# Kernel tuning notes

Hardware: AMD Instinct MI355X
Metric: run time of the kernel (lower is better)

Reference implementation:

```python
import jax, jax.numpy as jnp
import numpy as np

T, B, E, H, V, L = 128, 64, 1024, 1024, 10000, 2


def setup_inputs() -> dict:
    key = jax.random.key(0)
    ks = jax.random.split(key, 10)
    k = 1.0 / np.sqrt(H)
    u = lambda kk, shape, a: jax.random.uniform(kk, shape, jnp.float32, -a, a)
    return {
        "emb_table": u(ks[0], (V, E), 0.1),
        "W_in0": u(ks[1], (H, E), k),   # first layer input weight (no bias in linear_W)
        "Wh0": u(ks[2], (H, H), k),
        "b0": u(ks[3], (H,), k),
        "W_in1": u(ks[4], (H, H), k),
        "Wh1": u(ks[5], (H, H), k),
        "b1": u(ks[6], (H,), k),
        "Wdec": u(ks[7], (V, H), 0.1),
        "bdec": jnp.zeros((V,), jnp.float32),
        "hidden": jnp.zeros((L, B, H), jnp.float32),
        "tokens": jax.random.randint(ks[8], (T, B), 0, V, jnp.int32),
    }


def reference(emb_table, W_in0, Wh0, b0, W_in1, Wh1, b1, Wdec, bdec, hidden, tokens):
    # dp_keep_prob = 1.0 -> dropout is identity
    x_emb = emb_table[tokens]  # [T, B, E]

    def step(h, x):
        # h: [L, B, H]; x: [B, E]
        h0 = jnp.tanh(x @ W_in0.T + h[0] @ Wh0.T + b0)
        h1 = jnp.tanh(h0 @ W_in1.T + h[1] @ Wh1.T + b1)
        logits_t = h1 @ Wdec.T + bdec  # [B, V]
        return jnp.stack([h0, h1]), logits_t

    h_final, logits = jax.lax.scan(step, hidden, x_emb)
    return logits, h_final  # [T, B, V], [L, B, H]
```

## Files before the change

kernel.cpp:

```cpp
#include <hip/hip_runtime.h>
#include <hip/hip_bf16.h>
#include <stdint.h>

typedef __bf16 bf16_t;
typedef __bf16 bf16x8 __attribute__((ext_vector_type(8)));
typedef __bf16 bf16x4 __attribute__((ext_vector_type(4)));
typedef float  floatx4 __attribute__((ext_vector_type(4)));

#define T_STEPS 128
#define BATCH   64
#define EDIM    1024
#define HDIM    1024
#define VOCAB   10000
#define MROWS   (T_STEPS * BATCH)
#define RNN_BLOCKS 128
#define BH      (BATCH * HDIM)

__device__ __forceinline__ floatx4 mfma16(bf16x8 a, bf16x8 b, floatx4 c) {
    return __builtin_amdgcn_mfma_f32_16x16x32_bf16(a, b, c, 0, 0, 0);
}

__device__ __forceinline__ void gl_lds16(const bf16_t* g, bf16_t* l) {
    __builtin_amdgcn_global_load_lds(
        (const __attribute__((address_space(1))) void*)g,
        (__attribute__((address_space(3))) void*)l, 16, 0, 0);
}

__device__ __forceinline__ void store_bf16_bypass(bf16_t* p, float v) {
    union { bf16_t b; unsigned short u; } cv;
    cv.b = (bf16_t)v;
    unsigned int d = cv.u;
    asm volatile("global_store_short %0, %1, off sc0 sc1"
                 :: "v"(p), "v"(d) : "memory");
}


__global__ void f2b_kernel(const float* __restrict__ s, bf16_t* __restrict__ d, int n) {
    int i = (blockIdx.x * blockDim.x + threadIdx.x) * 4;
    if (i < n) {
        float4 v = *(const float4*)(s + i);
        bf16x4 o;
        o.x = (bf16_t)v.x; o.y = (bf16_t)v.y; o.z = (bf16_t)v.z; o.w = (bf16_t)v.w;
        *(bf16x4*)(d + i) = o;
    }
}

__global__ void gather_kernel(const float* __restrict__ emb, const int* __restrict__ tok,
                              bf16_t* __restrict__ X) {
    int row = blockIdx.x;
    int t = tok[row];
    int e = threadIdx.x * 4;
    float4 v = *(const float4*)(emb + (size_t)t * EDIM + e);
    bf16x4 o;
    o.x = (bf16_t)v.x; o.y = (bf16_t)v.y; o.z = (bf16_t)v.z; o.w = (bf16_t)v.w;
    *(bf16x4*)(X + (size_t)row * EDIM + e) = o;
}

__global__ void init_state_kernel(const float* __restrict__ hidden,
                                  bf16_t* __restrict__ h0all, bf16_t* __restrict__ h1all,
                                  int* __restrict__ flags) {
    int i = blockIdx.x * blockDim.x + threadIdx.x;
    h0all[i] = (bf16_t)hidden[i];
    h1all[i] = (bf16_t)hidden[BATCH * HDIM + i];
    if (i < 128) flags[i] = 0;
}


template <int OUT_BF16>
__global__ __launch_bounds__(256) void gemm_kernel(
    const bf16_t* __restrict__ A, const bf16_t* __restrict__ W,
    const float* __restrict__ bias, void* __restrict__ out,
    int M, int N, int K)
{
    const int tid  = threadIdx.x;
    const int lane = tid & 63;
    const int wave = tid >> 6;
    const int wm   = wave & 1;
    const int wn   = wave >> 1;
    const int quad = lane >> 4;
    const int l16  = lane & 15;
    const int mTile = blockIdx.y * 128;
    const int nTile = blockIdx.x * 128;

    __shared__ __align__(16) bf16_t sA[128 * 32];
    __shared__ __align__(16) bf16_t sW[128 * 32];

    const floatx4 fzero = {0.f, 0.f, 0.f, 0.f};
    floatx4 acc[4][4];
    #pragma unroll
    for (int i = 0; i < 4; ++i)
        #pragma unroll
        for (int j = 0; j < 4; ++j) acc[i][j] = fzero;

    for (int kk = 0; kk < K; kk += 32) {
        __syncthreads();
        #pragma unroll
        for (int j = 0; j < 2; ++j) {
            int c   = tid + j * 256;
            int row = c >> 2;
            int sub = c & 3;
            gl_lds16(A + (size_t)(mTile + row) * K + kk + sub * 8, sA + c * 8);
            int wrow = nTile + row;
            if (wrow >= N) wrow = N - 1;
            gl_lds16(W + (size_t)wrow * K + kk + sub * 8, sW + c * 8);
        }
        __syncthreads();
        bf16x8 af[4], wf[4];
        #pragma unroll
        for (int mi = 0; mi < 4; ++mi)
            af[mi] = *(const bf16x8*)(sA + (wm * 64 + mi * 16 + l16) * 32 + quad * 8);
        #pragma unroll
        for (int ni = 0; ni < 4; ++ni)
            wf[ni] = *(const bf16x8*)(sW + (wn * 64 + ni * 16 + l16) * 32 + quad * 8);
        #pragma unroll
        for (int mi = 0; mi < 4; ++mi)
            #pragma unroll
            for (int ni = 0; ni < 4; ++ni)
                acc[mi][ni] = mfma16(af[mi], wf[ni], acc[mi][ni]);
    }

    #pragma unroll
    for (int ni = 0; ni < 4; ++ni) {
        int col = nTile + wn * 64 + ni * 16 + l16;
        if (col < N) {
            float bv = bias[col];
            #pragma unroll
            for (int mi = 0; mi < 4; ++mi) {
                #pragma unroll
                for (int r = 0; r < 4; ++r) {
                    int row = mTile + wm * 64 + mi * 16 + quad * 4 + r;
                    float v = acc[mi][ni][r] + bv;
                    if (OUT_BF16) ((bf16_t*)out)[(size_t)row * N + col] = (bf16_t)v;
                    else          ((float*)out)[(size_t)row * N + col] = v;
                }
            }
        }
    }
}


__global__ __launch_bounds__(256, 1) void rnn_step_kernel(
    const bf16_t* __restrict__ X0,
    const bf16_t* __restrict__ Wh0b,
    const bf16_t* __restrict__ Win1b,
    const bf16_t* __restrict__ Wh1b,
    const float*  __restrict__ b1,
    bf16_t* __restrict__ h0all,
    bf16_t* __restrict__ h1all,
    int* __restrict__ flags)
{
    __shared__ __align__(16) char smem[65536];
    const int tid  = threadIdx.x;
    const int lane = tid & 63;
    const int wave = tid >> 6;
    const int quad = lane >> 4;
    const int l16  = lane & 15;
    const bool isL1 = blockIdx.x >= 64;
    const int cb    = blockIdx.x & 63;
    const int cbase = cb * 16;
    const int colg  = cbase + l16;
    const int arow  = (wave * 16 + l16) * HDIM;
    const int orow0 = wave * 16 + quad * 4;
    const floatx4 fzero = {0.f, 0.f, 0.f, 0.f};
    int* f0 = flags;
    int* f1 = flags + 64;

    {
        const bf16_t* W0 = isL1 ? Win1b : Wh0b;
        for (int c = tid; c < 2048; c += 256) {
            int kc2 = c >> 6, ln = c & 63;
            const bf16_t* src = W0 + (size_t)(cbase + (ln & 15)) * HDIM + kc2 * 32 + (ln >> 4) * 8;
            *(int4*)(smem + c * 16) = *(const int4*)src;
        }
        if (isL1) {
            for (int c = tid; c < 2048; c += 256) {
                int kc2 = c >> 6, ln = c & 63;
                const bf16_t* src = Wh1b + (size_t)(cbase + (ln & 15)) * HDIM + kc2 * 32 + (ln >> 4) * 8;
                *(int4*)(smem + 32768 + c * 16) = *(const int4*)src;
            }
        }
    }
    __syncthreads();

    if (!isL1) {
        float xr[4];
        #pragma unroll
        for (int r = 0; r < 4; ++r)
            xr[r] = (float)X0[(size_t)(orow0 + r) * HDIM + colg];
        int vc = 0;
        for (int t = 0; t < T_STEPS; ++t) {
            if (t > 0) {
                if (wave == 0) {
                    while (!__all(vc >= t)) {
                        if (vc < t)
                            vc = __hip_atomic_load(&f0[lane], __ATOMIC_RELAXED,
                                                   __HIP_MEMORY_SCOPE_AGENT);
                    }
                }
                __syncthreads();
            }
            const bf16_t* Ap = h0all + (size_t)t * BH;
            bf16x8 av[32];
            #pragma unroll
            for (int kc = 0; kc < 32; ++kc)
                av[kc] = *(const bf16x8*)(Ap + arow + kc * 32 + quad * 8);
            float xn[4];
            if (t + 1 < T_STEPS) {
                #pragma unroll
                for (int r = 0; r < 4; ++r)
                    xn[r] = (float)X0[((size_t)(t + 1) * BATCH + orow0 + r) * HDIM + colg];
            }
            floatx4 a0 = fzero, a1 = fzero;
            #pragma unroll
            for (int kc = 0; kc < 32; ++kc) {
                bf16x8 wv = *(const bf16x8*)(smem + kc * 1024 + lane * 16);
                if (kc & 1) a1 = mfma16(av[kc], wv, a1);
                else        a0 = mfma16(av[kc], wv, a0);
            }
            bf16_t* dst = h0all + (size_t)(t + 1) * BH;
            #pragma unroll
            for (int r = 0; r < 4; ++r)
                store_bf16_bypass(dst + (size_t)(orow0 + r) * HDIM + colg,
                                  tanhf(xr[r] + a0[r] + a1[r]));
            #pragma unroll
            for (int r = 0; r < 4; ++r) xr[r] = xn[r];
            asm volatile("s_waitcnt vmcnt(0)" ::: "memory");
            __syncthreads();
            if (tid == 0)
                __hip_atomic_store(&f0[cb], t + 1, __ATOMIC_RELAXED,
                                   __HIP_MEMORY_SCOPE_AGENT);
        }
    } else {
        const float bb = b1[colg];
        int vc0 = 0, vc1 = 0;
        for (int t = 0; t < T_STEPS; ++t) {
            if (wave == 0) {
                while (!__all(vc0 >= t + 1)) {
                    if (vc0 < t + 1)
                        vc0 = __hip_atomic_load(&f0[lane], __ATOMIC_RELAXED,
                                                __HIP_MEMORY_SCOPE_AGENT);
                }
            }
            __syncthreads();
            const bf16_t* A0 = h0all + (size_t)(t + 1) * BH;
            bf16x8 av0[32];
            #pragma unroll
            for (int kc = 0; kc < 32; ++kc)
                av0[kc] = *(const bf16x8*)(A0 + arow + kc * 32 + quad * 8);
            floatx4 aA = fzero, aB = fzero;
            #pragma unroll
            for (int kc = 0; kc < 32; ++kc) {
                bf16x8 wv1 = *(const bf16x8*)(smem + kc * 1024 + lane * 16);
                if (kc & 1) aB = mfma16(av0[kc], wv1, aB);
                else        aA = mfma16(av0[kc], wv1, aA);
            }
            if (t > 0) {
                if (wave == 0) {
                    while (!__all(vc1 >= t)) {
                        if (vc1 < t)
                            vc1 = __hip_atomic_load(&f1[lane], __ATOMIC_RELAXED,
                                                    __HIP_MEMORY_SCOPE_AGENT);
                    }
                }
                __syncthreads();
            }
            const bf16_t* A1 = h1all + (size_t)t * BH;
            bf16x8 av1[32];
            #pragma unroll
            for (int kc = 0; kc < 32; ++kc)
                av1[kc] = *(const bf16x8*)(A1 + arow + kc * 32 + quad * 8);
            #pragma unroll
            for (int kc = 0; kc < 32; ++kc) {
                bf16x8 wv2 = *(const bf16x8*)(smem + 32768 + kc * 1024 + lane * 16);
                if (kc & 1) aB = mfma16(av1[kc], wv2, aB);
                else        aA = mfma16(av1[kc], wv2, aA);
            }
            bf16_t* dst = h1all + (size_t)(t + 1) * BH;
            #pragma unroll
            for (int r = 0; r < 4; ++r)
                store_bf16_bypass(dst + (size_t)(orow0 + r) * HDIM + colg,
                                  tanhf(aA[r] + aB[r] + bb));
            asm volatile("s_waitcnt vmcnt(0)" ::: "memory");
            __syncthreads();
            if (tid == 0)
                __hip_atomic_store(&f1[cb], t + 1, __ATOMIC_RELAXED,
                                   __HIP_MEMORY_SCOPE_AGENT);
        }
    }
}

__global__ void finalize_kernel(const bf16_t* __restrict__ h0all,
                                const bf16_t* __restrict__ h1all,
                                float* __restrict__ out) {
    int i = blockIdx.x * blockDim.x + threadIdx.x;
    const size_t OUT0 = (size_t)MROWS * VOCAB;
    out[OUT0 + i]                = (float)h0all[(size_t)T_STEPS * BATCH * HDIM + i];
    out[OUT0 + BATCH * HDIM + i] = (float)h1all[(size_t)T_STEPS * BATCH * HDIM + i];
}


extern "C" void kernel_launch(void* const* d_in, const int* in_sizes, int n_in,
                              void* d_out, int out_size, void* d_ws, size_t ws_size,
                              hipStream_t stream) {
    (void)in_sizes; (void)n_in; (void)out_size; (void)ws_size;
    const float* emb    = (const float*)d_in[0];
    const float* W_in0  = (const float*)d_in[1];
    const float* Wh0    = (const float*)d_in[2];
    const float* b0     = (const float*)d_in[3];
    const float* W_in1  = (const float*)d_in[4];
    const float* Wh1    = (const float*)d_in[5];
    const float* b1     = (const float*)d_in[6];
    const float* Wdec   = (const float*)d_in[7];
    const float* bdec   = (const float*)d_in[8];
    const float* hidden = (const float*)d_in[9];
    const int*   tokens = (const int*)d_in[10];
    float* out = (float*)d_out;

    char* ws = (char*)d_ws;
    auto alloc = [&](size_t bytes) {
        char* p = ws; ws += (bytes + 255) & ~(size_t)255; return p;
    };
    bf16_t* Xemb  = (bf16_t*)alloc((size_t)MROWS * EDIM * 2);
    bf16_t* X0    = (bf16_t*)alloc((size_t)MROWS * HDIM * 2);
    bf16_t* Win0b = (bf16_t*)alloc((size_t)HDIM * EDIM * 2);
    bf16_t* Wh0b  = (bf16_t*)alloc((size_t)HDIM * HDIM * 2);
    bf16_t* Win1b = (bf16_t*)alloc((size_t)HDIM * HDIM * 2);
    bf16_t* Wh1b  = (bf16_t*)alloc((size_t)HDIM * HDIM * 2);
    bf16_t* Wdecb = (bf16_t*)alloc((size_t)VOCAB * HDIM * 2);
    bf16_t* h1all = (bf16_t*)alloc((size_t)(T_STEPS + 1) * BATCH * HDIM * 2);
    bf16_t* h0all = (bf16_t*)alloc((size_t)(T_STEPS + 1) * BATCH * HDIM * 2);
    int*    flags = (int*)alloc(512);

    f2b_kernel<<<dim3(HDIM * EDIM / 1024), 256, 0, stream>>>(W_in0, Win0b, HDIM * EDIM);
    f2b_kernel<<<dim3(HDIM * HDIM / 1024), 256, 0, stream>>>(Wh0,   Wh0b,  HDIM * HDIM);
    f2b_kernel<<<dim3(HDIM * HDIM / 1024), 256, 0, stream>>>(W_in1, Win1b, HDIM * HDIM);
    f2b_kernel<<<dim3(HDIM * HDIM / 1024), 256, 0, stream>>>(Wh1,   Wh1b,  HDIM * HDIM);
    f2b_kernel<<<dim3(VOCAB * HDIM / 1024), 256, 0, stream>>>(Wdec, Wdecb, VOCAB * HDIM);
    gather_kernel<<<dim3(MROWS), 256, 0, stream>>>(emb, tokens, Xemb);
    init_state_kernel<<<dim3(256), 256, 0, stream>>>(hidden, h0all, h1all, flags);

    gemm_kernel<1><<<dim3(HDIM / 128, MROWS / 128), 256, 0, stream>>>(
        Xemb, Win0b, b0, X0, MROWS, HDIM, EDIM);

    rnn_step_kernel<<<dim3(RNN_BLOCKS), 256, 0, stream>>>(
        X0, Wh0b, Win1b, Wh1b, b1, h0all, h1all, flags);

    gemm_kernel<0><<<dim3((VOCAB + 127) / 128, MROWS / 128), 256, 0, stream>>>(
        h1all + BATCH * HDIM, Wdecb, bdec, out, MROWS, VOCAB, HDIM);

    finalize_kernel<<<dim3(256), 256, 0, stream>>>(h0all, h1all, out);
}
```

Before: 1.801 ms.

## Merge RNN layer blocks into skewed wavefront with one flag per phase

Replaces the 128-block split (64 blocks for layer 0, 64 for layer 1, each with its own flag array) with 64 blocks. Each block computes layer 0 for step p and layer 1 for step p-1 in the same phase, so all three recurrent weight slices sit in 96KB of LDS. The goal is to halve the inter-block barrier waits per step and to reuse the loaded h0 tile for both layers. It also pads the flags to one per 64-byte line and adds s_sleep to the spin loop to cut contention. In exchange each block does twice the MFMA work per phase on half as many CUs, which lengthens the per-phase critical path.

Measured after the change: 2.032 ms. 12.8% more time.

```diff
diff --git a/kernel.cpp b/kernel.cpp
--- a/kernel.cpp
+++ b/kernel.cpp
@@ -13,8 +13,9 @@
 #define HDIM    1024
 #define VOCAB   10000
 #define MROWS   (T_STEPS * BATCH)
-#define RNN_BLOCKS 128
+#define RNN_BLOCKS 64
 #define BH      (BATCH * HDIM)
+#define FSTRIDE 16
 
 __device__ __forceinline__ floatx4 mfma16(bf16x8 a, bf16x8 b, floatx4 c) {
     return __builtin_amdgcn_mfma_f32_16x16x32_bf16(a, b, c, 0, 0, 0);
@@ -62,7 +63,7 @@
     int i = blockIdx.x * blockDim.x + threadIdx.x;
     h0all[i] = (bf16_t)hidden[i];
     h1all[i] = (bf16_t)hidden[BATCH * HDIM + i];
-    if (i < 128) flags[i] = 0;
+    if (i < 128 * FSTRIDE) flags[i] = 0;
 }
 
 
@@ -149,143 +150,118 @@
     bf16_t* __restrict__ h1all,
     int* __restrict__ flags)
 {
-    __shared__ __align__(16) char smem[65536];
+    __shared__ __align__(16) char smem[98304];
     const int tid  = threadIdx.x;
     const int lane = tid & 63;
     const int wave = tid >> 6;
     const int quad = lane >> 4;
     const int l16  = lane & 15;
-    const bool isL1 = blockIdx.x >= 64;
-    const int cb    = blockIdx.x & 63;
+    const int cb    = blockIdx.x;
     const int cbase = cb * 16;
     const int colg  = cbase + l16;
     const int arow  = (wave * 16 + l16) * HDIM;
     const int orow0 = wave * 16 + quad * 4;
     const floatx4 fzero = {0.f, 0.f, 0.f, 0.f};
-    int* f0 = flags;
-    int* f1 = flags + 64;
 
     {
-        const bf16_t* W0 = isL1 ? Win1b : Wh0b;
-        for (int c = tid; c < 2048; c += 256) {
-            int kc2 = c >> 6, ln = c & 63;
-            const bf16_t* src = W0 + (size_t)(cbase + (ln & 15)) * HDIM + kc2 * 32 + (ln >> 4) * 8;
-            *(int4*)(smem + c * 16) = *(const int4*)src;
-        }
-        if (isL1) {
+        #pragma unroll
+        for (int s = 0; s < 3; ++s) {
+            const bf16_t* Ws = (s == 0) ? Wh0b : (s == 1) ? Win1b : Wh1b;
             for (int c = tid; c < 2048; c += 256) {
                 int kc2 = c >> 6, ln = c & 63;
-                const bf16_t* src = Wh1b + (size_t)(cbase + (ln & 15)) * HDIM + kc2 * 32 + (ln >> 4) * 8;
-                *(int4*)(smem + 32768 + c * 16) = *(const int4*)src;
+                const bf16_t* src = Ws + (size_t)(cbase + (ln & 15)) * HDIM + kc2 * 32 + (ln >> 4) * 8;
+                *(int4*)(smem + s * 32768 + c * 16) = *(const int4*)src;
             }
         }
     }
     __syncthreads();
 
-    if (!isL1) {
-        float xr[4];
-        #pragma unroll
-        for (int r = 0; r < 4; ++r)
-            xr[r] = (float)X0[(size_t)(orow0 + r) * HDIM + colg];
-        int vc = 0;
-        for (int t = 0; t < T_STEPS; ++t) {
-            if (t > 0) {
-                if (wave == 0) {
-                    while (!__all(vc >= t)) {
-                        if (vc < t)
-                            vc = __hip_atomic_load(&f0[lane], __ATOMIC_RELAXED,
-                                                   __HIP_MEMORY_SCOPE_AGENT);
+    const float bb = b1[colg];
+
+    float xr[4];
+    #pragma unroll
+    for (int r = 0; r < 4; ++r)
+        xr[r] = (float)X0[(size_t)(orow0 + r) * HDIM + colg];
+
+    int vc = 0;
+    for (int p = 0; p <= T_STEPS; ++p) {
+        if (p > 0) {
+            if (wave == 0) {
+                while (!__all(vc >= p)) {
+                    if (vc < p) {
+                        vc = __hip_atomic_load(&flags[lane * FSTRIDE], __ATOMIC_RELAXED,
+                                               __HIP_MEMORY_SCOPE_AGENT);
+                        if (vc < p) __builtin_amdgcn_s_sleep(1);
                     }
                 }
-                __syncthreads();
-            }
-            const bf16_t* Ap = h0all + (size_t)t * BH;
-            bf16x8 av[32];
-            #pragma unroll
-            for (int kc = 0; kc < 32; ++kc)
-                av[kc] = *(const bf16x8*)(Ap + arow + kc * 32 + quad * 8);
+            }
+            __syncthreads();
+        }
+
+        const bf16_t* A0 = h0all + (size_t)p * BH;
+        bf16x8 av0[32];
+        #pragma unroll
+        for (int kc = 0; kc < 32; ++kc)
+            av0[kc] = *(const bf16x8*)(A0 + arow + kc * 32 + quad * 8);
+
+        if (p < T_STEPS) {
             float xn[4];
-            if (t + 1 < T_STEPS) {
+            if (p + 1 < T_STEPS) {
                 #pragma unroll
                 for (int r = 0; r < 4; ++r)
-                    xn[r] = (float)X0[((size_t)(t + 1) * BATCH + orow0 + r) * HDIM + colg];
+                    xn[r] = (float)X0[((size_t)(p + 1) * BATCH + orow0 + r) * HDIM + colg];
             }
             floatx4 a0 = fzero, a1 = fzero;
             #pragma unroll
             for (int kc = 0; kc < 32; ++kc) {
                 bf16x8 wv = *(const bf16x8*)(smem + kc * 1024 + lane * 16);
-                if (kc & 1) a1 = mfma16(av[kc], wv, a1);
-                else        a0 = mfma16(av[kc], wv, a0);
-            }
-            bf16_t* dst = h0all + (size_t)(t + 1) * BH;
+                if (kc & 1) a1 = mfma16(av0[kc], wv, a1);
+                else        a0 = mfma16(av0[kc], wv, a0);
+            }
+            bf16_t* dst = h0all + (size_t)(p + 1) * BH;
             #pragma unroll
             for (int r = 0; r < 4; ++r)
                 store_bf16_bypass(dst + (size_t)(orow0 + r) * HDIM + colg,
                                   tanhf(xr[r] + a0[r] + a1[r]));
-            #pragma unroll
-            for (int r = 0; r < 4; ++r) xr[r] = xn[r];
-            asm volatile("s_waitcnt vmcnt(0)" ::: "memory");
-            __syncthreads();
-            if (tid == 0)
-                __hip_atomic_store(&f0[cb], t + 1, __ATOMIC_RELAXED,
-                                   __HIP_MEMORY_SCOPE_AGENT);
-        }
-    } else {
-        const float bb = b1[colg];
-        int vc0 = 0, vc1 = 0;
-        for (int t = 0; t < T_STEPS; ++t) {
-            if (wave == 0) {
-                while (!__all(vc0 >= t + 1)) {
-                    if (vc0 < t + 1)
-                        vc0 = __hip_atomic_load(&f0[lane], __ATOMIC_RELAXED,
-                                                __HIP_MEMORY_SCOPE_AGENT);
-                }
-            }
-            __syncthreads();
-            const bf16_t* A0 = h0all + (size_t)(t + 1) * BH;
-            bf16x8 av0[32];
+            if (p + 1 < T_STEPS) {
+                #pragma unroll
+                for (int r = 0; r < 4; ++r) xr[r] = xn[r];
+            }
+        }
+
+        if (p >= 1) {
+            const bf16_t* A1 = h1all + (size_t)(p - 1) * BH;
+            bf16x8 av1[32];
             #pragma unroll
             for (int kc = 0; kc < 32; ++kc)
-                av0[kc] = *(const bf16x8*)(A0 + arow + kc * 32 + quad * 8);
+                av1[kc] = *(const bf16x8*)(A1 + arow + kc * 32 + quad * 8);
             floatx4 aA = fzero, aB = fzero;
             #pragma unroll
             for (int kc = 0; kc < 32; ++kc) {
-                bf16x8 wv1 = *(const bf16x8*)(smem + kc * 1024 + lane * 16);
+                bf16x8 wv1 = *(const bf16x8*)(smem + 32768 + kc * 1024 + lane * 16);
                 if (kc & 1) aB = mfma16(av0[kc], wv1, aB);
                 else        aA = mfma16(av0[kc], wv1, aA);
             }
-            if (t > 0) {
-                if (wave == 0) {
-                    while (!__all(vc1 >= t)) {
-                        if (vc1 < t)
-                            vc1 = __hip_atomic_load(&f1[lane], __ATOMIC_RELAXED,
-                                                    __HIP_MEMORY_SCOPE_AGENT);
-                    }
-                }
-                __syncthreads();
-            }
-            const bf16_t* A1 = h1all + (size_t)t * BH;
-            bf16x8 av1[32];
-            #pragma unroll
-            for (int kc = 0; kc < 32; ++kc)
-                av1[kc] = *(const bf16x8*)(A1 + arow + kc * 32 + quad * 8);
             #pragma unroll
             for (int kc = 0; kc < 32; ++kc) {
-                bf16x8 wv2 = *(const bf16x8*)(smem + 32768 + kc * 1024 + lane * 16);
+                bf16x8 wv2 = *(const bf16x8*)(smem + 65536 + kc * 1024 + lane * 16);
                 if (kc & 1) aB = mfma16(av1[kc], wv2, aB);
                 else        aA = mfma16(av1[kc], wv2, aA);
             }
-            bf16_t* dst = h1all + (size_t)(t + 1) * BH;
+            bf16_t* dst = h1all + (size_t)p * BH;
             #pragma unroll
             for (int r = 0; r < 4; ++r)
                 store_bf16_bypass(dst + (size_t)(orow0 + r) * HDIM + colg,
                                   tanhf(aA[r] + aB[r] + bb));
-            asm volatile("s_waitcnt vmcnt(0)" ::: "memory");
-            __syncthreads();
-            if (tid == 0)
-                __hip_atomic_store(&f1[cb], t + 1, __ATOMIC_RELAXED,
-                                   __HIP_MEMORY_SCOPE_AGENT);
-        }
+        }
+
+        if (p == T_STEPS) break;
+
+        asm volatile("s_waitcnt vmcnt(0)" ::: "memory");
+        __syncthreads();
+        if (tid == 0)
+            __hip_atomic_store(&flags[cb * FSTRIDE], p + 1, __ATOMIC_RELAXED,
+                               __HIP_MEMORY_SCOPE_AGENT);
     }
 }
 
@@ -329,7 +305,7 @@
     bf16_t* Wdecb = (bf16_t*)alloc((size_t)VOCAB * HDIM * 2);
     bf16_t* h1all = (bf16_t*)alloc((size_t)(T_STEPS + 1) * BATCH * HDIM * 2);
     bf16_t* h0all = (bf16_t*)alloc((size_t)(T_STEPS + 1) * BATCH * HDIM * 2);
-    int*    flags = (int*)alloc(512);
+    int*    flags = (int*)alloc(128 * FSTRIDE * 4);
 
     f2b_kernel<<<dim3(HDIM * EDIM / 1024), 256, 0, stream>>>(W_in0, Win0b, HDIM * EDIM);
     f2b_kernel<<<dim3(HDIM * HDIM / 1024), 256, 0, stream>>>(Wh0,   Wh0b,  HDIM * HDIM);
```
